# Kernel optimization log

Measured on AMD Instinct MI355X. Metric: run time of the kernel, lower is better.

## Reference

```python
import jax, jax.numpy as jnp
import numpy as np

K = 3          # kernel size
PAD = 1        # padding
# deformable conv v2: offset conv (2*K*K ch), modulator conv (K*K ch, 2*sigmoid), main 3x3 conv, ReLU


def _conv2d(x, w, b):
    y = jax.lax.conv_general_dilated(x, w, (1, 1), ((PAD, PAD), (PAD, PAD)),
                                     dimension_numbers=('NCHW', 'OIHW', 'NCHW'))
    return y + b[None, :, None, None]


def _bilinear_gather(x, py, px):
    # x: [B,C,H,W]; py/px: [B,K2,H,W] float sample coords; zero outside image.
    B, C, H, W = x.shape
    y0 = jnp.floor(py)
    x0 = jnp.floor(px)
    wy1 = py - y0
    wx1 = px - x0
    wy0 = 1.0 - wy1
    wx0 = 1.0 - wx1
    xf = x.reshape(B, C, H * W)

    def gather(yi, xi):
        valid = (yi >= 0) & (yi <= H - 1) & (xi >= 0) & (xi <= W - 1)
        yc = jnp.clip(yi, 0, H - 1).astype(jnp.int32)
        xc = jnp.clip(xi, 0, W - 1).astype(jnp.int32)
        idx = (yc * W + xc).reshape(B, -1)                      # [B, K2*H*W]
        v = jax.vmap(lambda xb, ib: xb[:, ib])(xf, idx)         # [B, C, K2*H*W]
        v = v.reshape(B, C, *yi.shape[1:])                      # [B, C, K2, H, W]
        return v * valid[:, None].astype(x.dtype)

    return (gather(y0, x0) * (wy0 * wx0)[:, None]
            + gather(y0, x0 + 1) * (wy0 * wx1)[:, None]
            + gather(y0 + 1, x0) * (wy1 * wx0)[:, None]
            + gather(y0 + 1, x0 + 1) * (wy1 * wx1)[:, None])


def _deform_conv(data, w, b, w_off, b_off, w_mod, b_mod):
    B, Cin, H, W = data.shape
    off = _conv2d(data, w_off, b_off)                           # [B, 2*K2, H, W]
    mask = 2.0 * jax.nn.sigmoid(_conv2d(data, w_mod, b_mod))    # [B, K2, H, W]
    off = off.reshape(B, K * K, 2, H, W)                        # (dy, dx) per tap
    dy, dx = off[:, :, 0], off[:, :, 1]
    ki, kj = jnp.meshgrid(jnp.arange(K), jnp.arange(K), indexing='ij')
    ki = ki.reshape(-1).astype(data.dtype)
    kj = kj.reshape(-1).astype(data.dtype)
    hs = jnp.arange(H, dtype=data.dtype)
    ws = jnp.arange(W, dtype=data.dtype)
    py = hs[None, None, :, None] - PAD + ki[None, :, None, None] + dy
    px = ws[None, None, None, :] - PAD + kj[None, :, None, None] + dx
    sampled = _bilinear_gather(data, py, px)                    # [B, Cin, K2, H, W]
    sampled = sampled * mask[:, None]
    out = jnp.einsum('bckhw,ock->bohw', sampled, w.reshape(w.shape[0], Cin, K * K))
    return out + b[None, :, None, None]


def setup_inputs() -> dict:
    key = jax.random.key(0)
    ks = jax.random.split(key, 7)
    B, Cin, Cout, H, W = 8, 64, 64, 128, 128
    fan = Cin * K * K
    return {
        'data': jax.random.normal(ks[0], (B, Cin, H, W), jnp.float32),
        'w': jax.random.normal(ks[1], (Cout, Cin, K, K), jnp.float32) / np.sqrt(fan),
        'b': jax.random.normal(ks[2], (Cout,), jnp.float32) * 0.01,
        'w_off': jax.random.normal(ks[3], (2 * K * K, Cin, K, K), jnp.float32) * (0.1 / np.sqrt(fan)),
        'b_off': jnp.zeros((2 * K * K,), jnp.float32),
        'w_mod': jax.random.normal(ks[4], (K * K, Cin, K, K), jnp.float32) * (0.1 / np.sqrt(fan)),
        'b_mod': jnp.zeros((K * K,), jnp.float32),
    }


def reference(data, w, b, w_off, b_off, w_mod, b_mod):
    return jax.nn.relu(_deform_conv(data, w, b, w_off, b_off, w_mod, b_mod))
```

## Files before the change

### kernel.cpp

```cpp
#include <hip/hip_runtime.h>
#include <hip/hip_fp16.h>
#include <cstdint>


typedef _Float16 half8 __attribute__((ext_vector_type(8)));
typedef __attribute__((ext_vector_type(4))) float floatx4;

__device__ __forceinline__ unsigned int pack2h(float lo, float hi) {
    __half2 h = __floats2half2_rn(lo, hi);
    union { __half2 h; unsigned int u; } cv; cv.h = h;
    return cv.u;
}
__device__ __forceinline__ unsigned int blend2h(unsigned int a, unsigned int b,
                                                unsigned int c, unsigned int d,
                                                const __half2* w) {
    union { unsigned int u; __half2 h; } A, B, C, D, O;
    A.u = a; B.u = b; C.u = c; D.u = d;
    __half2 s = __hmul2(A.h, w[0]);
    s = __hfma2(B.h, w[1], s);
    s = __hfma2(C.h, w[2], s);
    s = __hfma2(D.h, w[3], s);
    O.h = s;
    return O.u;
}

#define OFF_DATAT 0u
#define OFF_OFFP  16777216u
#define OFF_WM    30932992u
#define OFF_W27   31006720u
#define OFF_B27   31043584u

__global__ __launch_bounds__(256) void prep_k(const float* __restrict__ x,
                                              unsigned short* __restrict__ xt,
                                              const float* __restrict__ w,
                                              const float* __restrict__ w_off,
                                              const float* __restrict__ w_mod,
                                              const float* __restrict__ b_off,
                                              const float* __restrict__ b_mod,
                                              unsigned short* __restrict__ wpackM,
                                              unsigned short* __restrict__ wpack27,
                                              float* __restrict__ bias27) {
    __shared__ float tile[64][65];
    int blk = blockIdx.x;
    if (blk < 2048) {
        int b    = blk >> 8;
        int pos0 = (blk & 255) << 6;
        int lane = threadIdx.x & 63;
        int g    = threadIdx.x >> 6;
        for (int c = g; c < 64; c += 4)
            tile[c][lane] = x[(((b << 6) + c) << 14) + pos0 + lane];
        __syncthreads();
        int c2 = lane & 31;
        for (int i = g; i < 32; i += 4) {
            int pr = (i << 1) + (lane >> 5);
            unsigned int d = pack2h(tile[c2 << 1][pr], tile[(c2 << 1) + 1][pr]);
            *(unsigned int*)&xt[((size_t)((b << 14) + pos0 + pr) << 6) + (c2 << 1)] = d;
        }
        return;
    }
    int t = (blk - 2048) * 256 + threadIdx.x;
    if (t < 64 * 576) {
        int o = t / 576, kk = t % 576;
        int k = kk >> 6, c = kk & 63;
        wpackM[t] = __half_as_ushort(__float2half_rn(w[(o * 64 + c) * 9 + k]));
        return;
    }
    t -= 64 * 576;
    if (t < 32 * 576) {
        int o = t / 576, kk = t % 576;
        int k = kk >> 6, c = kk & 63;
        float v = 0.f;
        if (o < 18)      v = w_off[(o * 64 + c) * 9 + k];
        else if (o < 27) v = w_mod[((o - 18) * 64 + c) * 9 + k];
        wpack27[t] = __half_as_ushort(__float2half_rn(v));
        if (kk == 0) bias27[o] = (o < 18) ? b_off[o] : (o < 27 ? b_mod[o - 18] : 0.f);
    }
}

__global__ __launch_bounds__(256) void conv27_k(const unsigned short* __restrict__ xt,
                                                const unsigned short* __restrict__ wpack27,
                                                const float* __restrict__ bias27,
                                                float* __restrict__ offP) {
    __shared__ unsigned short tile[4][66][72];
    int blk   = blockIdx.x;
    int b     = blk >> 7;
    int patch = blk & 127;
    int m     = patch >> 1;
    int h     = patch & 1;
    int tid   = threadIdx.x;
    int lane  = tid & 63, wv = tid >> 6;
    int r = lane & 15, q = lane >> 4;

    const unsigned short* xb = xt + ((size_t)b << 20);

    {
        int g = tid >> 3, j = tid & 7;
        #pragma unroll
        for (int rr = 0; rr < 4; ++rr) {
            int sy = (m << 1) + rr - 1;
            #pragma unroll
            for (int ci = 0; ci < 3; ++ci) {
                int col = g + (ci << 5);
                if (col < 66) {
                    int sx = (h << 6) + col - 1;
                    uint4 v = {0u, 0u, 0u, 0u};
                    if (sy >= 0 && sy < 128 && sx >= 0 && sx < 128)
                        v = *(const uint4*)&xb[(size_t)(((sy << 7) + sx) << 6) + (j << 3)];
                    *(uint4*)&tile[rr][col][j << 3] = v;
                }
            }
        }
    }
    __syncthreads();

    floatx4 acc[4] = {};
    #pragma unroll
    for (int k = 0; k < 9; ++k) {
        int ki = k / 3, kj = k % 3;
        #pragma unroll
        for (int ch = 0; ch < 2; ++ch) {
            half8 a0 = *(const half8*)&wpack27[(r)      * 576 + (k << 6) + (ch << 5) + (q << 3)];
            half8 a1 = *(const half8*)&wpack27[(16 + r) * 576 + (k << 6) + (ch << 5) + (q << 3)];
            #pragma unroll
            for (int tr = 0; tr < 2; ++tr) {
                half8 bfrag = *(const half8*)&tile[tr + ki][(wv << 4) + r + kj][(ch << 5) + (q << 3)];
                acc[0 + tr] = __builtin_amdgcn_mfma_f32_16x16x32_f16(a0, bfrag, acc[0 + tr], 0, 0, 0);
                acc[2 + tr] = __builtin_amdgcn_mfma_f32_16x16x32_f16(a1, bfrag, acc[2 + tr], 0, 0, 0);
            }
        }
    }

    #pragma unroll
    for (int s = 0; s < 2; ++s) {
        #pragma unroll
        for (int tr = 0; tr < 2; ++tr) {
            #pragma unroll
            for (int reg = 0; reg < 4; ++reg) {
                int oc = (s << 4) + (q << 2) + reg;
                if (oc >= 27) continue;
                int pos = (((m << 1) + tr) << 7) + (h << 6) + (wv << 4) + r;
                float v = acc[(s << 1) + tr][reg] + bias27[oc];
                int kk, comp;
                if (oc < 18) { kk = oc >> 1; comp = oc & 1; }
                else         { kk = oc - 18; comp = 2; v = 2.f / (1.f + __expf(-v)); }
                offP[(size_t)(((b * 9 + kk) * 3 + comp) << 14) + pos] = v;
            }
        }
    }
}

__global__ __launch_bounds__(256, 3) void deform_main_k(const unsigned short* __restrict__ xt,
                                                        const unsigned short* __restrict__ wpackM,
                                                        const float* __restrict__ offP,
                                                        const float* __restrict__ bias,
                                                        float* __restrict__ out) {
    __shared__ ushort4 pOff[576];
    __shared__ uint4   pW[576];
    __shared__ unsigned short samp[2][64][72];
    int blk  = blockIdx.x;
    int b    = blk >> 8;
    int pos0 = (blk & 255) << 6;
    int tid  = threadIdx.x;
    int lane = tid & 63, wv = tid >> 6;
    int r = lane & 15, q = lane >> 4;
    int pg = lane >> 3;
    int j8 = lane & 7;

    const char* xbb = (const char*)(xt + ((size_t)b << 20));

    for (int e = tid; e < 576; e += 256) {
        int k = e >> 6, p = e & 63;
        int pos = pos0 + p;
        const float* offk = offP + ((size_t)((b * 9 + k) * 3) << 14);
        float dy = offk[pos];
        float dx = offk[16384 + pos];
        float m  = offk[32768 + pos];
        float py = (float)(pos >> 7) + (float)(k / 3 - 1) + dy;
        float px = (float)(pos & 127) + (float)(k % 3 - 1) + dx;
        float y0f = floorf(py), x0f = floorf(px);
        int y0 = (int)y0f, x0 = (int)x0f;
        float wy1 = py - y0f, wx1 = px - x0f;
        float wy0 = 1.f - wy1, wx0 = 1.f - wx1;
        bool vy0 = (y0 >= 0) && (y0 < 128);
        bool vy1 = (y0 >= -1) && (y0 < 127);
        bool vx0 = (x0 >= 0) && (x0 < 128);
        bool vx1 = (x0 >= -1) && (x0 < 127);
        float w00 = (vy0 && vx0) ? m * wy0 * wx0 : 0.f;
        float w01 = (vy0 && vx1) ? m * wy0 * wx1 : 0.f;
        float w10 = (vy1 && vx0) ? m * wy1 * wx0 : 0.f;
        float w11 = (vy1 && vx1) ? m * wy1 * wx1 : 0.f;
        int y0c = min(max(y0, 0), 127), y1c = min(max(y0 + 1, 0), 127);
        int x0c = min(max(x0, 0), 127), x1c = min(max(x0 + 1, 0), 127);
        ushort4 io;
        io.x = (unsigned short)((y0c << 7) + x0c);
        io.y = (unsigned short)((y0c << 7) + x1c);
        io.z = (unsigned short)((y1c << 7) + x0c);
        io.w = (unsigned short)((y1c << 7) + x1c);
        pOff[e] = io;
        union { uint4 u; __half2 h[4]; } pw;
        pw.h[0] = __float2half2_rn(w00);
        pw.h[1] = __float2half2_rn(w01);
        pw.h[2] = __float2half2_rn(w10);
        pw.h[3] = __float2half2_rn(w11);
        pW[e] = pw.u;
    }
    __syncthreads();

    floatx4 acc[4] = {};
    const char* xp = xbb + (j8 << 4);
    const unsigned short* wrow = wpackM + ((wv << 4) + r) * 576 + (q << 3);

    uint4   c00[2][2], c01[2][2], c10[2][2], c11[2][2];
    uint4   cwS[2][2];
    ushort4 nio[2];
    uint4   ncw[2];
    half8   afC[2], afN[2];

    auto readParams = [&](int k) {
        #pragma unroll
        for (int i = 0; i < 2; ++i) {
            int e  = (k << 6) + (wv << 4) + (i << 3) + pg;
            nio[i] = pOff[e];
            ncw[i] = pW[e];
        }
    };
    auto issueInto = [&](int s) {
        #pragma unroll
        for (int i = 0; i < 2; ++i) {
            cwS[s][i] = ncw[i];
            c00[s][i] = *(const uint4*)(xp + ((int)nio[i].x << 7));
            c01[s][i] = *(const uint4*)(xp + ((int)nio[i].y << 7));
            c10[s][i] = *(const uint4*)(xp + ((int)nio[i].z << 7));
            c11[s][i] = *(const uint4*)(xp + ((int)nio[i].w << 7));
        }
    };
    auto blendStore = [&](int s, int buf) {
        #pragma unroll
        for (int i = 0; i < 2; ++i) {
            int p = (wv << 4) + (i << 3) + pg;
            union { uint4 u; __half2 h[4]; } W; W.u = cwS[s][i];
            uint4 o4;
            o4.x = blend2h(c00[s][i].x, c01[s][i].x, c10[s][i].x, c11[s][i].x, W.h);
            o4.y = blend2h(c00[s][i].y, c01[s][i].y, c10[s][i].y, c11[s][i].y, W.h);
            o4.z = blend2h(c00[s][i].z, c01[s][i].z, c10[s][i].z, c11[s][i].z, W.h);
            o4.w = blend2h(c00[s][i].w, c01[s][i].w, c10[s][i].w, c11[s][i].w, W.h);
            *(uint4*)&samp[buf][p][j8 << 3] = o4;
        }
    };

    auto ldsBarrier = [&]() {
        asm volatile("s_waitcnt lgkmcnt(0)\n\ts_barrier" ::: "memory");
    };

    readParams(0); issueInto(0);
    readParams(1); issueInto(1);
    afC[0] = *(const half8*)&wrow[0];
    afC[1] = *(const half8*)&wrow[32];
    blendStore(0, 0);
    readParams(2);

    #pragma unroll
    for (int k = 0; k < 9; ++k) {
        if (k <= 6) issueInto(k & 1);
        if (k < 8) {
            afN[0] = *(const half8*)&wrow[((k + 1) << 6)];
            afN[1] = *(const half8*)&wrow[((k + 1) << 6) + 32];
        }
        ldsBarrier();
        #pragma unroll
        for (int ch = 0; ch < 2; ++ch) {
            #pragma unroll
            for (int nt = 0; nt < 4; ++nt) {
                half8 bfrag = *(const half8*)&samp[k & 1][(nt << 4) + r][(ch << 5) + (q << 3)];
                acc[nt] = __builtin_amdgcn_mfma_f32_16x16x32_f16(afC[ch], bfrag, acc[nt], 0, 0, 0);
            }
        }
        if (k < 8) {
            blendStore((k + 1) & 1, (k + 1) & 1);
            if (k <= 5) readParams(k + 3);
            afC[0] = afN[0];
            afC[1] = afN[1];
        }
    }

    #pragma unroll
    for (int nt = 0; nt < 4; ++nt) {
        #pragma unroll
        for (int reg = 0; reg < 4; ++reg) {
            int oc  = (wv << 4) + (q << 2) + reg;
            int pos = pos0 + (nt << 4) + r;
            float v = acc[nt][reg] + bias[oc];
            out[(size_t)(((b << 6) + oc) << 14) + pos] = fmaxf(v, 0.f);
        }
    }
}

extern "C" void kernel_launch(void* const* d_in, const int* in_sizes, int n_in,
                              void* d_out, int out_size, void* d_ws, size_t ws_size,
                              hipStream_t stream) {
    const float* data  = (const float*)d_in[0];
    const float* w     = (const float*)d_in[1];
    const float* bias  = (const float*)d_in[2];
    const float* w_off = (const float*)d_in[3];
    const float* b_off = (const float*)d_in[4];
    const float* w_mod = (const float*)d_in[5];
    const float* b_mod = (const float*)d_in[6];
    float* out = (float*)d_out;

    char* ws = (char*)d_ws;
    unsigned short* dataT   = (unsigned short*)(ws + OFF_DATAT);
    float*          offP    = (float*)(ws + OFF_OFFP);
    unsigned short* wpackM  = (unsigned short*)(ws + OFF_WM);
    unsigned short* wpack27 = (unsigned short*)(ws + OFF_W27);
    float*          bias27  = (float*)(ws + OFF_B27);

    prep_k<<<2264, 256, 0, stream>>>(data, dataT, w, w_off, w_mod,
                                     b_off, b_mod, wpackM, wpack27, bias27);
    conv27_k<<<1024, 256, 0, stream>>>(dataT, wpack27, bias27, offP);
    deform_main_k<<<2048, 256, 0, stream>>>(dataT, wpackM, offP, bias, out);
}
```

Baseline: 162.9 us.

## Fuse offset/modulator conv into deform main kernel via shared LDS

Removes the separate conv27 kernel and computes the 27-channel offset/mask conv inside each deform_main block for its 64 positions, keeping results in LDS instead of a global offP buffer. This cuts a kernel launch and the global write and read of the offset tensor. LDS is aliased between the conv tile and the later sampling buffers. In exchange, the halo input rows are loaded per block with less reuse (one row per block instead of two), and LDS pressure could affect occupancy.

```diff
diff --git a/kernel.cpp b/kernel.cpp
--- a/kernel.cpp
+++ b/kernel.cpp
@@ -25,10 +25,9 @@
 }
 
 #define OFF_DATAT 0u
-#define OFF_OFFP  16777216u
-#define OFF_WM    30932992u
-#define OFF_W27   31006720u
-#define OFF_B27   31043584u
+#define OFF_WM    16777216u
+#define OFF_W27   16850944u
+#define OFF_B27   16887808u
 
 __global__ __launch_bounds__(256) void prep_k(const float* __restrict__ x,
                                               unsigned short* __restrict__ xt,
@@ -77,86 +76,19 @@
     }
 }
 
-__global__ __launch_bounds__(256) void conv27_k(const unsigned short* __restrict__ xt,
-                                                const unsigned short* __restrict__ wpack27,
-                                                const float* __restrict__ bias27,
-                                                float* __restrict__ offP) {
-    __shared__ unsigned short tile[4][66][72];
-    int blk   = blockIdx.x;
-    int b     = blk >> 7;
-    int patch = blk & 127;
-    int m     = patch >> 1;
-    int h     = patch & 1;
-    int tid   = threadIdx.x;
-    int lane  = tid & 63, wv = tid >> 6;
-    int r = lane & 15, q = lane >> 4;
-
-    const unsigned short* xb = xt + ((size_t)b << 20);
-
-    {
-        int g = tid >> 3, j = tid & 7;
-        #pragma unroll
-        for (int rr = 0; rr < 4; ++rr) {
-            int sy = (m << 1) + rr - 1;
-            #pragma unroll
-            for (int ci = 0; ci < 3; ++ci) {
-                int col = g + (ci << 5);
-                if (col < 66) {
-                    int sx = (h << 6) + col - 1;
-                    uint4 v = {0u, 0u, 0u, 0u};
-                    if (sy >= 0 && sy < 128 && sx >= 0 && sx < 128)
-                        v = *(const uint4*)&xb[(size_t)(((sy << 7) + sx) << 6) + (j << 3)];
-                    *(uint4*)&tile[rr][col][j << 3] = v;
-                }
-            }
-        }
-    }
-    __syncthreads();
-
-    floatx4 acc[4] = {};
-    #pragma unroll
-    for (int k = 0; k < 9; ++k) {
-        int ki = k / 3, kj = k % 3;
-        #pragma unroll
-        for (int ch = 0; ch < 2; ++ch) {
-            half8 a0 = *(const half8*)&wpack27[(r)      * 576 + (k << 6) + (ch << 5) + (q << 3)];
-            half8 a1 = *(const half8*)&wpack27[(16 + r) * 576 + (k << 6) + (ch << 5) + (q << 3)];
-            #pragma unroll
-            for (int tr = 0; tr < 2; ++tr) {
-                half8 bfrag = *(const half8*)&tile[tr + ki][(wv << 4) + r + kj][(ch << 5) + (q << 3)];
-                acc[0 + tr] = __builtin_amdgcn_mfma_f32_16x16x32_f16(a0, bfrag, acc[0 + tr], 0, 0, 0);
-                acc[2 + tr] = __builtin_amdgcn_mfma_f32_16x16x32_f16(a1, bfrag, acc[2 + tr], 0, 0, 0);
-            }
-        }
-    }
-
-    #pragma unroll
-    for (int s = 0; s < 2; ++s) {
-        #pragma unroll
-        for (int tr = 0; tr < 2; ++tr) {
-            #pragma unroll
-            for (int reg = 0; reg < 4; ++reg) {
-                int oc = (s << 4) + (q << 2) + reg;
-                if (oc >= 27) continue;
-                int pos = (((m << 1) + tr) << 7) + (h << 6) + (wv << 4) + r;
-                float v = acc[(s << 1) + tr][reg] + bias27[oc];
-                int kk, comp;
-                if (oc < 18) { kk = oc >> 1; comp = oc & 1; }
-                else         { kk = oc - 18; comp = 2; v = 2.f / (1.f + __expf(-v)); }
-                offP[(size_t)(((b * 9 + kk) * 3 + comp) << 14) + pos] = v;
-            }
-        }
-    }
-}
-
 __global__ __launch_bounds__(256, 3) void deform_main_k(const unsigned short* __restrict__ xt,
                                                         const unsigned short* __restrict__ wpackM,
-                                                        const float* __restrict__ offP,
+                                                        const unsigned short* __restrict__ wpack27,
+                                                        const float* __restrict__ bias27,
                                                         const float* __restrict__ bias,
                                                         float* __restrict__ out) {
-    __shared__ ushort4 pOff[576];
-    __shared__ uint4   pW[576];
-    __shared__ unsigned short samp[2][64][72];
+    __shared__ __align__(16) char ldsbuf[35680];
+    ushort4*        pOff   = (ushort4*)(ldsbuf);
+    uint4*          pW     = (uint4*)(ldsbuf + 4608);
+    unsigned short (*samp)[64][72]   = (unsigned short (*)[64][72])(ldsbuf + 13824);
+    unsigned short (*tile27)[66][72] = (unsigned short (*)[66][72])(ldsbuf);
+    float          (*pp)[28]         = (float (*)[28])(ldsbuf + 28512);
+
     int blk  = blockIdx.x;
     int b    = blk >> 8;
     int pos0 = (blk & 255) << 6;
@@ -166,15 +98,60 @@
     int pg = lane >> 3;
     int j8 = lane & 7;
 
-    const char* xbb = (const char*)(xt + ((size_t)b << 20));
+    const unsigned short* xb = xt + ((size_t)b << 20);
+    const char* xbb = (const char*)xb;
+
+    {
+        int row = pos0 >> 7;
+        int c0  = pos0 & 127;
+        for (int e = tid; e < 1584; e += 256) {
+            int rr  = e / 528;
+            int rem = e - rr * 528;
+            int cc  = rem >> 3;
+            int j   = rem & 7;
+            int sy  = row - 1 + rr;
+            int sx  = c0 - 1 + cc;
+            uint4 v = {0u, 0u, 0u, 0u};
+            if (sy >= 0 && sy < 128 && sx >= 0 && sx < 128)
+                v = *(const uint4*)&xb[(size_t)(((sy << 7) + sx) << 6) + (j << 3)];
+            *(uint4*)&tile27[rr][cc][j << 3] = v;
+        }
+        __syncthreads();
+
+        floatx4 acc27[2] = {};
+        #pragma unroll
+        for (int k = 0; k < 9; ++k) {
+            int ki = k / 3, kj = k % 3;
+            #pragma unroll
+            for (int chh = 0; chh < 2; ++chh) {
+                half8 a0 = *(const half8*)&wpack27[(r)      * 576 + (k << 6) + (chh << 5) + (q << 3)];
+                half8 a1 = *(const half8*)&wpack27[(16 + r) * 576 + (k << 6) + (chh << 5) + (q << 3)];
+                half8 bf = *(const half8*)&tile27[ki][(wv << 4) + r + kj][(chh << 5) + (q << 3)];
+                acc27[0] = __builtin_amdgcn_mfma_f32_16x16x32_f16(a0, bf, acc27[0], 0, 0, 0);
+                acc27[1] = __builtin_amdgcn_mfma_f32_16x16x32_f16(a1, bf, acc27[1], 0, 0, 0);
+            }
+        }
+        #pragma unroll
+        for (int s = 0; s < 2; ++s) {
+            #pragma unroll
+            for (int reg = 0; reg < 4; ++reg) {
+                int oc = (s << 4) + (q << 2) + reg;
+                if (oc < 27) {
+                    float v = acc27[s][reg] + bias27[oc];
+                    if (oc >= 18) v = 2.f / (1.f + __expf(-v));
+                    pp[(wv << 4) + r][oc] = v;
+                }
+            }
+        }
+        __syncthreads();
+    }
 
     for (int e = tid; e < 576; e += 256) {
         int k = e >> 6, p = e & 63;
         int pos = pos0 + p;
-        const float* offk = offP + ((size_t)((b * 9 + k) * 3) << 14);
-        float dy = offk[pos];
-        float dx = offk[16384 + pos];
-        float m  = offk[32768 + pos];
+        float dy = pp[p][(k << 1)];
+        float dx = pp[p][(k << 1) + 1];
+        float m  = pp[p][18 + k];
         float py = (float)(pos >> 7) + (float)(k / 3 - 1) + dy;
         float px = (float)(pos & 127) + (float)(k % 3 - 1) + dx;
         float y0f = floorf(py), x0f = floorf(px);
@@ -309,13 +286,11 @@
 
     char* ws = (char*)d_ws;
     unsigned short* dataT   = (unsigned short*)(ws + OFF_DATAT);
-    float*          offP    = (float*)(ws + OFF_OFFP);
     unsigned short* wpackM  = (unsigned short*)(ws + OFF_WM);
     unsigned short* wpack27 = (unsigned short*)(ws + OFF_W27);
     float*          bias27  = (float*)(ws + OFF_B27);
 
     prep_k<<<2264, 256, 0, stream>>>(data, dataT, w, w_off, w_mod,
                                      b_off, b_mod, wpackM, wpack27, bias27);
-    conv27_k<<<1024, 256, 0, stream>>>(dataT, wpack27, bias27, offP);
-    deform_main_k<<<2048, 256, 0, stream>>>(dataT, wpackM, offP, bias, out);
-}
+    deform_main_k<<<2048, 256, 0, stream>>>(dataT, wpackM, wpack27, bias27, bias, out);
+}
```

Result: slower. 169.5 us (+4.0%).

## Drop LDS staging in offset conv; read fragments directly from global with prepacked weights

Applied to the files above, without the earlier changes.

The offset/modulator conv kernel no longer stages a halo tile in shared memory behind a barrier. Each lane now loads its B fragment straight from the channel-last fp16 input, relying on the L1/L2 caches for reuse across the 3x3 taps. The A weights are also repacked in the prep kernel into lane-contiguous fragment order, so each half8 weight load is coalesced across the wavefront. The trade-off is more global and cache traffic and per-load bounds checks in exchange for removing the LDS writes and the synchronisation.

```diff
diff --git a/kernel.cpp b/kernel.cpp
--- a/kernel.cpp
+++ b/kernel.cpp
@@ -38,7 +38,7 @@
                                               const float* __restrict__ b_off,
                                               const float* __restrict__ b_mod,
                                               unsigned short* __restrict__ wpackM,
-                                              unsigned short* __restrict__ wpack27,
+                                              unsigned short* __restrict__ wq,
                                               float* __restrict__ bias27) {
     __shared__ float tile[64][65];
     int blk = blockIdx.x;
@@ -72,16 +72,18 @@
         float v = 0.f;
         if (o < 18)      v = w_off[(o * 64 + c) * 9 + k];
         else if (o < 27) v = w_mod[((o - 18) * 64 + c) * 9 + k];
-        wpack27[t] = __half_as_ushort(__float2half_rn(v));
+        int s = o >> 4, r = o & 15;
+        int chh = c >> 5, q = (c >> 3) & 3, j = c & 7;
+        int dst = (((((k << 1) + chh) << 1) + s) << 9) + (q << 7) + (r << 3) + j;
+        wq[dst] = __half_as_ushort(__float2half_rn(v));
         if (kk == 0) bias27[o] = (o < 18) ? b_off[o] : (o < 27 ? b_mod[o - 18] : 0.f);
     }
 }
 
 __global__ __launch_bounds__(256) void conv27_k(const unsigned short* __restrict__ xt,
-                                                const unsigned short* __restrict__ wpack27,
+                                                const unsigned short* __restrict__ wq,
                                                 const float* __restrict__ bias27,
                                                 float* __restrict__ offP) {
-    __shared__ unsigned short tile[4][66][72];
     int blk   = blockIdx.x;
     int b     = blk >> 7;
     int patch = blk & 127;
@@ -92,40 +94,28 @@
     int r = lane & 15, q = lane >> 4;
 
     const unsigned short* xb = xt + ((size_t)b << 20);
-
-    {
-        int g = tid >> 3, j = tid & 7;
-        #pragma unroll
-        for (int rr = 0; rr < 4; ++rr) {
-            int sy = (m << 1) + rr - 1;
-            #pragma unroll
-            for (int ci = 0; ci < 3; ++ci) {
-                int col = g + (ci << 5);
-                if (col < 66) {
-                    int sx = (h << 6) + col - 1;
-                    uint4 v = {0u, 0u, 0u, 0u};
-                    if (sy >= 0 && sy < 128 && sx >= 0 && sx < 128)
-                        v = *(const uint4*)&xb[(size_t)(((sy << 7) + sx) << 6) + (j << 3)];
-                    *(uint4*)&tile[rr][col][j << 3] = v;
-                }
-            }
-        }
-    }
-    __syncthreads();
+    int rb  = (m << 1) - 1;
+    int cxb = (h << 6) + (wv << 4) + r - 1;
+    int chq = (q << 3);
 
     floatx4 acc[4] = {};
     #pragma unroll
     for (int k = 0; k < 9; ++k) {
         int ki = k / 3, kj = k % 3;
         #pragma unroll
-        for (int ch = 0; ch < 2; ++ch) {
-            half8 a0 = *(const half8*)&wpack27[(r)      * 576 + (k << 6) + (ch << 5) + (q << 3)];
-            half8 a1 = *(const half8*)&wpack27[(16 + r) * 576 + (k << 6) + (ch << 5) + (q << 3)];
+        for (int chh = 0; chh < 2; ++chh) {
+            int abase = ((((k << 1) + chh) << 1) << 9) + (lane << 3);
+            half8 a0 = *(const half8*)&wq[abase];
+            half8 a1 = *(const half8*)&wq[abase + 512];
             #pragma unroll
             for (int tr = 0; tr < 2; ++tr) {
-                half8 bfrag = *(const half8*)&tile[tr + ki][(wv << 4) + r + kj][(ch << 5) + (q << 3)];
-                acc[0 + tr] = __builtin_amdgcn_mfma_f32_16x16x32_f16(a0, bfrag, acc[0 + tr], 0, 0, 0);
-                acc[2 + tr] = __builtin_amdgcn_mfma_f32_16x16x32_f16(a1, bfrag, acc[2 + tr], 0, 0, 0);
+                int sy = rb + tr + ki;
+                int sx = cxb + kj;
+                half8 bf = {};
+                if ((unsigned)sy < 128u && (unsigned)sx < 128u)
+                    bf = *(const half8*)&xb[(size_t)(((sy << 7) + sx) << 6) + (chh << 5) + chq];
+                acc[0 + tr] = __builtin_amdgcn_mfma_f32_16x16x32_f16(a0, bf, acc[0 + tr], 0, 0, 0);
+                acc[2 + tr] = __builtin_amdgcn_mfma_f32_16x16x32_f16(a1, bf, acc[2 + tr], 0, 0, 0);
             }
         }
     }
@@ -311,11 +301,11 @@
     unsigned short* dataT   = (unsigned short*)(ws + OFF_DATAT);
     float*          offP    = (float*)(ws + OFF_OFFP);
     unsigned short* wpackM  = (unsigned short*)(ws + OFF_WM);
-    unsigned short* wpack27 = (unsigned short*)(ws + OFF_W27);
+    unsigned short* wq      = (unsigned short*)(ws + OFF_W27);
     float*          bias27  = (float*)(ws + OFF_B27);
 
     prep_k<<<2264, 256, 0, stream>>>(data, dataT, w, w_off, w_mod,
-                                     b_off, b_mod, wpackM, wpack27, bias27);
-    conv27_k<<<1024, 256, 0, stream>>>(dataT, wpack27, bias27, offP);
+                                     b_off, b_mod, wpackM, wq, bias27);
+    conv27_k<<<1024, 256, 0, stream>>>(dataT, wq, bias27, offP);
     deform_main_k<<<2048, 256, 0, stream>>>(dataT, wpackM, offP, bias, out);
 }
```

Measured after the change: 160.7 us. About the same (-1.4%).
